# Performance work log

Measured on AMD Instinct MI355X. Metric: run time of the kernel, lower is better.

## Reference

```python
import jax, jax.numpy as jnp
import numpy as np

B, S, D_IN = 2, 2048, 1024
HIDDEN, H, HKV = 1024, 16, 4
R = H // HKV          # query heads per kv head
HD = HIDDEN // H      # head_dim = 64
D_OUT = 1024
SCALE = HD ** -0.5


def setup_inputs() -> dict:
    key = jax.random.key(0)
    ks = jax.random.split(key, 5)
    x = jax.random.normal(ks[0], (B, S, D_IN), dtype=jnp.float32)
    # store weights as (in, out); torch Linear computes x @ W.T with W (out,in)
    Wq = jax.random.normal(ks[1], (D_IN, HIDDEN), dtype=jnp.float32) * 0.02
    Wk = jax.random.normal(ks[2], (D_IN, HKV * HD), dtype=jnp.float32) * 0.02
    Wv = jax.random.normal(ks[3], (D_IN, HKV * HD), dtype=jnp.float32) * 0.02
    Wo = jax.random.normal(ks[4], (HIDDEN, D_OUT), dtype=jnp.float32) * 0.02
    return {"x": x, "Wq": Wq, "Wk": Wk, "Wv": Wv, "Wo": Wo}


def reference(x, Wq, Wk, Wv, Wo):
    # projections
    q = x @ Wq                                   # (B,S,H*HD)
    k = x @ Wk                                   # (B,S,HKV*HD)
    v = x @ Wv
    # repeat_interleave maps query head h -> kv head h // R,
    # so split query heads as (HKV, R) groups and broadcast KV.
    q = q.reshape(B, S, HKV, R, HD)
    k = k.reshape(B, S, HKV, HD)
    v = v.reshape(B, S, HKV, HD)
    attn = jnp.einsum('bskrd,btkd->bkrst', q, k) * SCALE   # (B,HKV,R,S,S)
    attn = jax.nn.softmax(attn, axis=-1)
    o = jnp.einsum('bkrst,btkd->bskrd', attn, v)           # (B,S,HKV,R,HD)
    o = o.reshape(B, S, HIDDEN)
    return o @ Wo                                          # (B,S,D_OUT)
```

## Files before the change

### kernel.cpp

```cpp
#include <hip/hip_runtime.h>

using u16 = unsigned short;
using u32 = unsigned int;
typedef __bf16 bf16x8 __attribute__((ext_vector_type(8)));
typedef u16 u16x8 __attribute__((ext_vector_type(8)));
typedef u32 u32x2 __attribute__((ext_vector_type(2)));
typedef u32 u32x4 __attribute__((ext_vector_type(4)));
typedef float f32x4 __attribute__((ext_vector_type(4)));
typedef float f32x16 __attribute__((ext_vector_type(16)));

#define B_   2
#define S_   2048
#define DIN  1024
#define HID  1024
#define NH   16
#define NKV  4
#define HD_  64
#define QKVW 1536
#define QSCL 0.1803368801111244f

__device__ __forceinline__ u16 f2b(float f) {
  u32 u = __builtin_bit_cast(u32, f);
  u32 r = (u + 0x7FFFu + ((u >> 16) & 1u)) >> 16;
  return (u16)r;
}

__device__ __forceinline__ void gl16(const void* g, void* l) {
  __builtin_amdgcn_global_load_lds(
      (const __attribute__((address_space(1))) void*)g,
      (__attribute__((address_space(3))) void*)l, 16, 0, 0);
}

__global__ void k_cvt(const float* __restrict__ in, u16* __restrict__ out, int n8) {
  int i = blockIdx.x * 256 + threadIdx.x;
  if (i >= n8) return;
  const float4* p = (const float4*)(in + (size_t)i * 8);
  float4 a = p[0], b = p[1];
  u16x8 o;
  o[0] = f2b(a.x); o[1] = f2b(a.y); o[2] = f2b(a.z); o[3] = f2b(a.w);
  o[4] = f2b(b.x); o[5] = f2b(b.y); o[6] = f2b(b.z); o[7] = f2b(b.w);
  *(u16x8*)(out + (size_t)i * 8) = o;
}

__global__ __launch_bounds__(256) void k_cvt_t3(
    const float* __restrict__ Wq, const float* __restrict__ Wk,
    const float* __restrict__ Wv, u16* __restrict__ WT)
{
  __shared__ float t[32][33];
  const int k0 = blockIdx.x * 32, n0 = blockIdx.y * 32;
  const float* W; int N, nb;
  if (n0 < HID)             { W = Wq; N = HID; nb = n0; }
  else if (n0 < HID + 256)  { W = Wk; N = 256; nb = n0 - HID; }
  else                      { W = Wv; N = 256; nb = n0 - HID - 256; }
  const int c = threadIdx.x & 31, r8 = threadIdx.x >> 5;
#pragma unroll
  for (int i = 0; i < 4; ++i)
    t[r8 + i * 8][c] = W[(size_t)(k0 + r8 + i * 8) * N + nb + c];
  __syncthreads();
#pragma unroll
  for (int i = 0; i < 4; ++i)
    WT[(size_t)(n0 + r8 + i * 8) * DIN + k0 + c] = f2b(t[c][r8 + i * 8]);
}

__global__ __launch_bounds__(256) void k_cvt_t(const float* __restrict__ W, u16* __restrict__ WT, int K, int N) {
  __shared__ float t[32][33];
  const int k0 = blockIdx.x * 32, n0 = blockIdx.y * 32;
  const int c = threadIdx.x & 31, r8 = threadIdx.x >> 5;
#pragma unroll
  for (int i = 0; i < 4; ++i)
    t[r8 + i * 8][c] = W[(size_t)(k0 + r8 + i * 8) * N + n0 + c];
  __syncthreads();
#pragma unroll
  for (int i = 0; i < 4; ++i)
    WT[(size_t)(n0 + r8 + i * 8) * K + k0 + c] = f2b(t[c][r8 + i * 8]);
}

__global__ __launch_bounds__(256) void k_vt(const u16* __restrict__ QKV, u16* __restrict__ Vt) {
  __shared__ u16 t[32][33];
  const int s0 = blockIdx.x * 32;
  const int d0 = blockIdx.y * 32;
  const int z  = blockIdx.z;
  const int b = z >> 2, kv = z & 3;
  const int c = threadIdx.x & 31, r8 = threadIdx.x >> 5;
#pragma unroll
  for (int i = 0; i < 4; ++i)
    t[r8 + i * 8][c] = QKV[(size_t)(b * S_ + s0 + r8 + i * 8) * QKVW + (HID + NKV * HD_) + kv * HD_ + d0 + c];
  __syncthreads();
#pragma unroll
  for (int i = 0; i < 4; ++i)
    Vt[(size_t)(z * HD_ + d0 + r8 + i * 8) * S_ + s0 + c] = t[c][r8 + i * 8];
}

template <typename OutT>
__global__ __launch_bounds__(256, 4) void k_gemm_bt(
    const u16* __restrict__ A, const u16* __restrict__ Bt,
    OutT* __restrict__ C, int M, int N, int K, int scaleCols, float scl)
{
  __shared__ u16 lA[2][128 * 32];
  __shared__ u16 lB[2][64 * 32];
  const int tid  = threadIdx.x;
  const int lane = tid & 63;
  const int wave = tid >> 6;
  const int wm = wave >> 1, wn = wave & 1;
  const int g = lane >> 4, li = lane & 15;
  const int bm = blockIdx.y * 128, bn = blockIdx.x * 64;
  const int arow = wave * 16 + (lane >> 2);
  const int acol = (lane & 3) * 8;

  f32x4 acc[4][2];
#pragma unroll
  for (int i = 0; i < 4; ++i)
#pragma unroll
    for (int j = 0; j < 2; ++j) acc[i][j] = f32x4{0.f, 0.f, 0.f, 0.f};

  const u16* Ab = A + (size_t)bm * K;
  const u16* Bb = Bt + (size_t)bn * K;

  auto stage = [&](int k0, int buf) {
#pragma unroll
    for (int h = 0; h < 2; ++h)
      gl16(&Ab[(size_t)(h * 64 + arow) * K + k0 + acol], (char*)lA[buf] + h * 4096 + wave * 1024);
    gl16(&Bb[(size_t)arow * K + k0 + acol], (char*)lB[buf] + wave * 1024);
  };

  stage(0, 0);
  __syncthreads();

  int cur = 0;
  for (int k0 = 0; k0 < K; k0 += 32) {
    if (k0 + 32 < K) stage(k0 + 32, cur ^ 1);
    bf16x8 af[4], bfr[2];
#pragma unroll
    for (int mt = 0; mt < 4; ++mt)
      af[mt] = *(const bf16x8*)&lA[cur][(wm * 64 + mt * 16 + li) * 32 + g * 8];
#pragma unroll
    for (int nt = 0; nt < 2; ++nt)
      bfr[nt] = *(const bf16x8*)&lB[cur][(wn * 32 + nt * 16 + li) * 32 + g * 8];
    __builtin_amdgcn_s_setprio(1);
#pragma unroll
    for (int mt = 0; mt < 4; ++mt)
#pragma unroll
      for (int nt = 0; nt < 2; ++nt)
        acc[mt][nt] = __builtin_amdgcn_mfma_f32_16x16x32_bf16(af[mt], bfr[nt], acc[mt][nt], 0, 0, 0);
    __builtin_amdgcn_s_setprio(0);
    __syncthreads();
    cur ^= 1;
  }

#pragma unroll
  for (int mt = 0; mt < 4; ++mt)
#pragma unroll
    for (int nt = 0; nt < 2; ++nt)
#pragma unroll
      for (int r = 0; r < 4; ++r) {
        int row = bm + wm * 64 + mt * 16 + g * 4 + r;
        int col = bn + wn * 32 + nt * 16 + li;
        float v = acc[mt][nt][r];
        if (col < scaleCols) v *= scl;
        if constexpr (sizeof(OutT) == 4) C[(size_t)row * N + col] = v;
        else                             C[(size_t)row * N + col] = f2b(v);
      }
}

__global__ __launch_bounds__(256, 2) void k_attn(
    const u16* __restrict__ QKV, const u16* __restrict__ Vt_g, u16* __restrict__ O)
{
  __shared__ u16 K_lds[3][64 * 64];
  __shared__ u16 Vt_lds[3][64 * 64];
  const int tid  = threadIdx.x;
  const int lane = tid & 63;
  const int w    = tid >> 6;
  const int lq = lane & 31;
  const int hi = lane >> 5;
  const int swl = (lq & 7) << 3;
  const int hx = (hi * 8) ^ (swl & 8);
  const int s0 = blockIdx.x * 32;
  const int kv = blockIdx.y;
  const int b  = blockIdx.z;
  const int hq = kv * 4 + w;

  int dcol[4];
#pragma unroll
  for (int d0 = 0; d0 < 4; ++d0) dcol[d0] = (d0 * 16) ^ (swl & 48);

  bf16x8 qf[4];
  {
    const u16* qb = QKV + (size_t)(b * S_ + s0 + lq) * QKVW + hq * HD_ + hi * 8;
#pragma unroll
    for (int d0 = 0; d0 < 4; ++d0) qf[d0] = *(const bf16x8*)(qb + d0 * 16);
  }

  float l = 0.f;
  f32x16 oacc0 = {}, oacc1 = {};
  bf16x8 pa[4];

  const int sr8 = lane >> 3;
  const int scol = ((lane & 7) ^ sr8) * 8;
  const int srow = w * 16;
  const u16* kge = QKV + (size_t)(b * S_) * QKVW + HID + kv * HD_;
  const u16* vge = Vt_g + (size_t)((b * NKV + kv) * HD_) * S_;

  auto stage = [&](int t, int buf) {
#pragma unroll
    for (int h = 0; h < 2; ++h) {
      gl16(kge + (size_t)(t * 64 + srow + h * 8 + sr8) * QKVW + scol,
           (char*)K_lds[buf] + srow * 128 + h * 1024);
      gl16(vge + (size_t)(srow + h * 8 + sr8) * S_ + t * 64 + scol,
           (char*)Vt_lds[buf] + srow * 128 + h * 1024);
    }
  };

  stage(0, 0);
  __syncthreads();

#define PK(dst, x, y) asm("v_cvt_pk_bf16_f32 %0, %1, %2" : "=v"(dst) : "v"(x), "v"(y))
  constexpr int NT = S_ / 64;
  int cb = 0;
  for (int t = 0; t < NT; ++t) {
    int nb = cb + 1; if (nb == 3) nb = 0;
    int pb = cb - 1; if (pb < 0) pb = 2;
    if (t + 1 < NT) stage(t + 1, nb);

    f32x16 st0 = {}, st1 = {};
    const u16* Kc = K_lds[cb];
    __builtin_amdgcn_s_setprio(1);
#pragma unroll
    for (int d0 = 0; d0 < 4; ++d0) {
      bf16x8 kf0 = *(const bf16x8*)&Kc[lq * 64 + dcol[d0] + hx];
      bf16x8 kf1 = *(const bf16x8*)&Kc[(32 + lq) * 64 + dcol[d0] + hx];
      st0 = __builtin_amdgcn_mfma_f32_32x32x16_bf16(kf0, qf[d0], st0, 0, 0, 0);
      st1 = __builtin_amdgcn_mfma_f32_32x32x16_bf16(kf1, qf[d0], st1, 0, 0, 0);
    }

#pragma unroll
    for (int i = 0; i < 16; ++i) st0[i] = __builtin_amdgcn_exp2f(st0[i]);
#pragma unroll
    for (int i = 0; i < 16; ++i) st1[i] = __builtin_amdgcn_exp2f(st1[i]);
    float s8[8];
#pragma unroll
    for (int i = 0; i < 8; ++i)
      s8[i] = (st0[i] + st0[i + 8]) + (st1[i] + st1[i + 8]);
    s8[0] += s8[4]; s8[1] += s8[5]; s8[2] += s8[6]; s8[3] += s8[7];
    l += (s8[0] + s8[1]) + (s8[2] + s8[3]);

    if (t > 0) {
      const u16* Vc = Vt_lds[pb];
#pragma unroll
      for (int ks = 0; ks < 4; ++ks) {
        bf16x8 vf0 = *(const bf16x8*)&Vc[lq * 64 + dcol[ks] + hx];
        bf16x8 vf1 = *(const bf16x8*)&Vc[(32 + lq) * 64 + dcol[ks] + hx];
        oacc0 = __builtin_amdgcn_mfma_f32_32x32x16_bf16(pa[ks], vf0, oacc0, 0, 0, 0);
        oacc1 = __builtin_amdgcn_mfma_f32_32x32x16_bf16(pa[ks], vf1, oacc1, 0, 0, 0);
      }
    }
    __builtin_amdgcn_s_setprio(0);

#pragma unroll
    for (int kb2 = 0; kb2 < 2; ++kb2) {
      const f32x16& ev = kb2 ? st1 : st0;
      u32 a0, a1, b0, b1;
      u32x2 r0, r1;
      u32x4 wv;
      PK(a0, ev[0], ev[1]);  PK(a1, ev[2], ev[3]);
      PK(b0, ev[4], ev[5]);  PK(b1, ev[6], ev[7]);
      r0 = __builtin_amdgcn_permlane32_swap(a0, b0, false, false);
      r1 = __builtin_amdgcn_permlane32_swap(a1, b1, false, false);
      wv[0] = r0[0]; wv[1] = r1[0]; wv[2] = r0[1]; wv[3] = r1[1];
      pa[kb2 * 2] = __builtin_bit_cast(bf16x8, wv);
      PK(a0, ev[8],  ev[9]);  PK(a1, ev[10], ev[11]);
      PK(b0, ev[12], ev[13]); PK(b1, ev[14], ev[15]);
      r0 = __builtin_amdgcn_permlane32_swap(a0, b0, false, false);
      r1 = __builtin_amdgcn_permlane32_swap(a1, b1, false, false);
      wv[0] = r0[0]; wv[1] = r1[0]; wv[2] = r0[1]; wv[3] = r1[1];
      pa[kb2 * 2 + 1] = __builtin_bit_cast(bf16x8, wv);
    }

    __syncthreads();
    cb = nb;
  }
#undef PK

  {
    int pb = cb - 1; if (pb < 0) pb = 2;
    const u16* Vc = Vt_lds[pb];
    __builtin_amdgcn_s_setprio(1);
#pragma unroll
    for (int ks = 0; ks < 4; ++ks) {
      bf16x8 vf0 = *(const bf16x8*)&Vc[lq * 64 + dcol[ks] + hx];
      bf16x8 vf1 = *(const bf16x8*)&Vc[(32 + lq) * 64 + dcol[ks] + hx];
      oacc0 = __builtin_amdgcn_mfma_f32_32x32x16_bf16(pa[ks], vf0, oacc0, 0, 0, 0);
      oacc1 = __builtin_amdgcn_mfma_f32_32x32x16_bf16(pa[ks], vf1, oacc1, 0, 0, 0);
    }
    __builtin_amdgcn_s_setprio(0);
  }

  l += __shfl_xor(l, 32);
  const size_t obase = (size_t)(b * S_ + s0) * HID + hq * HD_ + lq;
#pragma unroll
  for (int r = 0; r < 16; ++r) {
    const int qrow = (r & 3) + 8 * (r >> 2) + 4 * hi;
    float lr = __shfl(l, qrow);
    float inv = __builtin_amdgcn_rcpf(lr);
    O[obase + (size_t)qrow * HID]      = f2b(oacc0[r] * inv);
    O[obase + (size_t)qrow * HID + 32] = f2b(oacc1[r] * inv);
  }
}

extern "C" void kernel_launch(void* const* d_in, const int* in_sizes, int n_in,
                              void* d_out, int out_size, void* d_ws, size_t ws_size,
                              hipStream_t stream) {
  (void)in_sizes; (void)n_in; (void)out_size; (void)ws_size;
  const float* x  = (const float*)d_in[0];
  const float* Wq = (const float*)d_in[1];
  const float* Wk = (const float*)d_in[2];
  const float* Wv = (const float*)d_in[3];
  const float* Wo = (const float*)d_in[4];
  float* out = (float*)d_out;

  const size_t M = (size_t)B_ * S_;
  u16* xb    = (u16*)d_ws;
  u16* WqkvT = xb    + M * DIN;
  u16* WoT   = WqkvT + (size_t)QKVW * DIN;
  u16* QKV   = WoT   + (size_t)HID * HID;
  u16* Ob    = QKV   + M * QKVW;
  u16* Vt    = Ob    + M * HID;

  k_cvt<<<dim3((int)(M * DIN / 8 / 256)), 256, 0, stream>>>(x, xb, (int)(M * DIN / 8));
  k_cvt_t3<<<dim3(DIN / 32, QKVW / 32), 256, 0, stream>>>(Wq, Wk, Wv, WqkvT);
  k_cvt_t<<<dim3(HID / 32, HID / 32),   256, 0, stream>>>(Wo, WoT, HID, HID);

  k_gemm_bt<u16><<<dim3(QKVW / 64, (int)(M / 128)), 256, 0, stream>>>(
      xb, WqkvT, QKV, (int)M, QKVW, DIN, HID, QSCL);

  k_vt<<<dim3(S_ / 32, HD_ / 32, B_ * NKV), 256, 0, stream>>>(QKV, Vt);

  k_attn<<<dim3(S_ / 32, NKV, B_), 256, 0, stream>>>(QKV, Vt, Ob);

  k_gemm_bt<float><<<dim3(HID / 64, (int)(M / 128)), 256, 0, stream>>>(
      Ob, WoT, out, (int)M, HID, HID, 0, 1.0f);
}
```

Baseline: 107.4 us.

## Merge prep kernels, write V transposed from QKV GEMM, remap blocks across XCDs

Folds the x conversion and the three weight transpose/convert kernels into a single prep launch. The V transpose kernel is removed: the QKV GEMM epilogue now writes V tiles directly in transposed layout. Both GEMMs and the attention kernel remap block IDs so that neighbouring tiles land on the same XCD, aiming for better L2 reuse. Together these cut launch count and one round trip of V through memory, at the cost of narrower, strided 8-byte stores for Vt.

Measured after the change: 100.4 us. 6.5% less time.

```diff
diff --git a/kernel.cpp b/kernel.cpp
--- a/kernel.cpp
+++ b/kernel.cpp
@@ -4,6 +4,7 @@
 using u32 = unsigned int;
 typedef __bf16 bf16x8 __attribute__((ext_vector_type(8)));
 typedef u16 u16x8 __attribute__((ext_vector_type(8)));
+typedef u16 u16x4 __attribute__((ext_vector_type(4)));
 typedef u32 u32x2 __attribute__((ext_vector_type(2)));
 typedef u32 u32x4 __attribute__((ext_vector_type(4)));
 typedef float f32x4 __attribute__((ext_vector_type(4)));
@@ -31,27 +32,32 @@
       (__attribute__((address_space(3))) void*)l, 16, 0, 0);
 }
 
-__global__ void k_cvt(const float* __restrict__ in, u16* __restrict__ out, int n8) {
-  int i = blockIdx.x * 256 + threadIdx.x;
-  if (i >= n8) return;
-  const float4* p = (const float4*)(in + (size_t)i * 8);
-  float4 a = p[0], b = p[1];
-  u16x8 o;
-  o[0] = f2b(a.x); o[1] = f2b(a.y); o[2] = f2b(a.z); o[3] = f2b(a.w);
-  o[4] = f2b(b.x); o[5] = f2b(b.y); o[6] = f2b(b.z); o[7] = f2b(b.w);
-  *(u16x8*)(out + (size_t)i * 8) = o;
-}
-
-__global__ __launch_bounds__(256) void k_cvt_t3(
-    const float* __restrict__ Wq, const float* __restrict__ Wk,
-    const float* __restrict__ Wv, u16* __restrict__ WT)
+__global__ __launch_bounds__(256) void k_prep(
+    const float* __restrict__ x, const float* __restrict__ Wq,
+    const float* __restrict__ Wk, const float* __restrict__ Wv,
+    const float* __restrict__ Wo,
+    u16* __restrict__ xb, u16* __restrict__ WqkvT, u16* __restrict__ WoT)
 {
   __shared__ float t[32][33];
-  const int k0 = blockIdx.x * 32, n0 = blockIdx.y * 32;
-  const float* W; int N, nb;
-  if (n0 < HID)             { W = Wq; N = HID; nb = n0; }
-  else if (n0 < HID + 256)  { W = Wk; N = 256; nb = n0 - HID; }
-  else                      { W = Wv; N = 256; nb = n0 - HID - 256; }
+  const int bid = blockIdx.x;
+  if (bid < 2048) {
+    const int i = bid * 256 + threadIdx.x;
+    const float4* p = (const float4*)(x + (size_t)i * 8);
+    float4 a = p[0], b = p[1];
+    u16x8 o;
+    o[0] = f2b(a.x); o[1] = f2b(a.y); o[2] = f2b(a.z); o[3] = f2b(a.w);
+    o[4] = f2b(b.x); o[5] = f2b(b.y); o[6] = f2b(b.z); o[7] = f2b(b.w);
+    *(u16x8*)(xb + (size_t)i * 8) = o;
+    return;
+  }
+  const int wid = bid - 2048;
+  const int k0 = (wid & 31) * 32;
+  const int n0 = (wid >> 5) * 32;
+  const float* W; int N, nb, drow; u16* dst;
+  if (n0 < HID)            { W = Wq; N = HID; nb = n0;              dst = WqkvT; drow = n0; }
+  else if (n0 < HID + 256) { W = Wk; N = 256; nb = n0 - HID;        dst = WqkvT; drow = n0; }
+  else if (n0 < QKVW)      { W = Wv; N = 256; nb = n0 - HID - 256;  dst = WqkvT; drow = n0; }
+  else                     { W = Wo; N = HID; nb = n0 - QKVW;       dst = WoT;   drow = n0 - QKVW; }
   const int c = threadIdx.x & 31, r8 = threadIdx.x >> 5;
 #pragma unroll
   for (int i = 0; i < 4; ++i)
@@ -59,51 +65,27 @@
   __syncthreads();
 #pragma unroll
   for (int i = 0; i < 4; ++i)
-    WT[(size_t)(n0 + r8 + i * 8) * DIN + k0 + c] = f2b(t[c][r8 + i * 8]);
-}
-
-__global__ __launch_bounds__(256) void k_cvt_t(const float* __restrict__ W, u16* __restrict__ WT, int K, int N) {
-  __shared__ float t[32][33];
-  const int k0 = blockIdx.x * 32, n0 = blockIdx.y * 32;
-  const int c = threadIdx.x & 31, r8 = threadIdx.x >> 5;
-#pragma unroll
-  for (int i = 0; i < 4; ++i)
-    t[r8 + i * 8][c] = W[(size_t)(k0 + r8 + i * 8) * N + n0 + c];
-  __syncthreads();
-#pragma unroll
-  for (int i = 0; i < 4; ++i)
-    WT[(size_t)(n0 + r8 + i * 8) * K + k0 + c] = f2b(t[c][r8 + i * 8]);
-}
-
-__global__ __launch_bounds__(256) void k_vt(const u16* __restrict__ QKV, u16* __restrict__ Vt) {
-  __shared__ u16 t[32][33];
-  const int s0 = blockIdx.x * 32;
-  const int d0 = blockIdx.y * 32;
-  const int z  = blockIdx.z;
-  const int b = z >> 2, kv = z & 3;
-  const int c = threadIdx.x & 31, r8 = threadIdx.x >> 5;
-#pragma unroll
-  for (int i = 0; i < 4; ++i)
-    t[r8 + i * 8][c] = QKV[(size_t)(b * S_ + s0 + r8 + i * 8) * QKVW + (HID + NKV * HD_) + kv * HD_ + d0 + c];
-  __syncthreads();
-#pragma unroll
-  for (int i = 0; i < 4; ++i)
-    Vt[(size_t)(z * HD_ + d0 + r8 + i * 8) * S_ + s0 + c] = t[c][r8 + i * 8];
+    dst[(size_t)(drow + r8 + i * 8) * DIN + k0 + c] = f2b(t[c][r8 + i * 8]);
 }
 
 template <typename OutT>
 __global__ __launch_bounds__(256, 4) void k_gemm_bt(
     const u16* __restrict__ A, const u16* __restrict__ Bt,
-    OutT* __restrict__ C, int M, int N, int K, int scaleCols, float scl)
+    OutT* __restrict__ C, int M, int N, int K, int scaleCols, float scl,
+    int gx, u16* __restrict__ VtOut)
 {
   __shared__ u16 lA[2][128 * 32];
   __shared__ u16 lB[2][64 * 32];
+  u32 wg = blockIdx.x;
+  const u32 cpx = gridDim.x >> 3;
+  wg = (wg & 7) * cpx + (wg >> 3);
+  const int bm = (int)(wg / (u32)gx) * 128, bn = (int)(wg % (u32)gx) * 64;
+
   const int tid  = threadIdx.x;
   const int lane = tid & 63;
   const int wave = tid >> 6;
   const int wm = wave >> 1, wn = wave & 1;
   const int g = lane >> 4, li = lane & 15;
-  const int bm = blockIdx.y * 128, bn = blockIdx.x * 64;
   const int arow = wave * 16 + (lane >> 2);
   const int acol = (lane & 3) * 8;
 
@@ -147,19 +129,37 @@
     cur ^= 1;
   }
 
-#pragma unroll
-  for (int mt = 0; mt < 4; ++mt)
-#pragma unroll
-    for (int nt = 0; nt < 2; ++nt)
-#pragma unroll
-      for (int r = 0; r < 4; ++r) {
-        int row = bm + wm * 64 + mt * 16 + g * 4 + r;
-        int col = bn + wn * 32 + nt * 16 + li;
-        float v = acc[mt][nt][r];
-        if (col < scaleCols) v *= scl;
-        if constexpr (sizeof(OutT) == 4) C[(size_t)row * N + col] = v;
-        else                             C[(size_t)row * N + col] = f2b(v);
+  const bool toVt = (VtOut != nullptr) && (bn >= HID + 256);
+  if (toVt) {
+    const int bofs = (bm >> 11) * 256;
+#pragma unroll
+    for (int mt = 0; mt < 4; ++mt) {
+      const int sbase = (bm & (S_ - 1)) + wm * 64 + mt * 16 + g * 4;
+#pragma unroll
+      for (int nt = 0; nt < 2; ++nt) {
+        const int col = bn + wn * 32 + nt * 16 + li;
+        const int vtrow = bofs + col - (HID + 256);
+        u16x4 pkv;
+#pragma unroll
+        for (int r = 0; r < 4; ++r) pkv[r] = f2b(acc[mt][nt][r]);
+        *(u16x4*)&VtOut[(size_t)vtrow * S_ + sbase] = pkv;
       }
+    }
+  } else {
+#pragma unroll
+    for (int mt = 0; mt < 4; ++mt)
+#pragma unroll
+      for (int nt = 0; nt < 2; ++nt)
+#pragma unroll
+        for (int r = 0; r < 4; ++r) {
+          int row = bm + wm * 64 + mt * 16 + g * 4 + r;
+          int col = bn + wn * 32 + nt * 16 + li;
+          float v = acc[mt][nt][r];
+          if (col < scaleCols) v *= scl;
+          if constexpr (sizeof(OutT) == 4) C[(size_t)row * N + col] = v;
+          else                             C[(size_t)row * N + col] = f2b(v);
+        }
+  }
 }
 
 __global__ __launch_bounds__(256, 2) void k_attn(
@@ -174,9 +174,10 @@
   const int hi = lane >> 5;
   const int swl = (lq & 7) << 3;
   const int hx = (hi * 8) ^ (swl & 8);
-  const int s0 = blockIdx.x * 32;
-  const int kv = blockIdx.y;
-  const int b  = blockIdx.z;
+  const int g8 = blockIdx.x & 7;
+  const int kv = g8 & 3;
+  const int b  = g8 >> 2;
+  const int s0 = (((int)blockIdx.z * 4 + (int)blockIdx.y) * 8 + ((int)blockIdx.x >> 3)) * 32;
   const int hq = kv * 4 + w;
 
   int dcol[4];
@@ -325,17 +326,13 @@
   u16* Ob    = QKV   + M * QKVW;
   u16* Vt    = Ob    + M * HID;
 
-  k_cvt<<<dim3((int)(M * DIN / 8 / 256)), 256, 0, stream>>>(x, xb, (int)(M * DIN / 8));
-  k_cvt_t3<<<dim3(DIN / 32, QKVW / 32), 256, 0, stream>>>(Wq, Wk, Wv, WqkvT);
-  k_cvt_t<<<dim3(HID / 32, HID / 32),   256, 0, stream>>>(Wo, WoT, HID, HID);
-
-  k_gemm_bt<u16><<<dim3(QKVW / 64, (int)(M / 128)), 256, 0, stream>>>(
-      xb, WqkvT, QKV, (int)M, QKVW, DIN, HID, QSCL);
-
-  k_vt<<<dim3(S_ / 32, HD_ / 32, B_ * NKV), 256, 0, stream>>>(QKV, Vt);
+  k_prep<<<dim3(4608), 256, 0, stream>>>(x, Wq, Wk, Wv, Wo, xb, WqkvT, WoT);
+
+  k_gemm_bt<u16><<<dim3(768), 256, 0, stream>>>(
+      xb, WqkvT, QKV, (int)M, QKVW, DIN, HID, QSCL, QKVW / 64, Vt);
 
   k_attn<<<dim3(S_ / 32, NKV, B_), 256, 0, stream>>>(QKV, Vt, Ob);
 
-  k_gemm_bt<float><<<dim3(HID / 64, (int)(M / 128)), 256, 0, stream>>>(
-      Ob, WoT, out, (int)M, HID, HID, 0, 1.0f);
-}
+  k_gemm_bt<float><<<dim3(512), 256, 0, stream>>>(
+      Ob, WoT, out, (int)M, HID, HID, 0, 1.0f, HID / 64, nullptr);
+}
```
